# Performance work log

Measured on AMD Instinct MI355X. Metric: run time of the kernel, lower is better.

The kernel has to match this reference:

```python
import jax, jax.numpy as jnp
import numpy as np

N, F, H, E, ES, G = 50000, 64, 4, 300000, 400000, 128
NS, EPS = 0.2, 1e-5  # LeakyReLU slope, BN eps


def setup_inputs() -> dict:
    k = jax.random.split(jax.random.key(0), 16)
    rn = lambda i, s, sc=1.0: jax.random.normal(k[i], s, jnp.float32) * sc
    return {
        "x": rn(0, (N, F)),
        "edge_index": jax.random.randint(k[1], (2, E), 0, N),
        "batch": jnp.sort(jax.random.randint(k[2], (N,), 0, G)),
        "scatter_edge_index": jax.random.randint(k[3], (4, 2, ES), 0, N),
        "scatter_edge_attr": rn(4, (4, ES), 0.1),
        "gat_W": rn(5, (4, F, H * F), 0.05),
        "gat_asrc": rn(6, (4, H, F), 0.05),
        "gat_adst": rn(7, (4, H, F), 0.05),
        "gat_bias": jnp.zeros((4, H * F)),
        "mlp_W": rn(8, (4, H * F, F), 0.05),
        "mlp_b": jnp.zeros((4, F)),
        "mlp_g": jnp.ones((4, F)), "mlp_beta": jnp.zeros((4, F)),
        "mlp_rm": jnp.zeros((4, F)), "mlp_rv": jax.random.uniform(k[9], (4, F)) + 0.5,
        "fc1_W": rn(10, (F, 256), 0.05), "fc1_b": jnp.zeros((256,)),
        "fc1_g": jnp.ones((256,)), "fc1_beta": jnp.zeros((256,)),
        "fc1_rm": jnp.zeros((256,)), "fc1_rv": jax.random.uniform(k[11], (256,)) + 0.5,
        "fc2_W": rn(12, (256, 64), 0.05), "fc2_b": jnp.zeros((64,)),
        "fc2_g": jnp.ones((64,)), "fc2_beta": jnp.zeros((64,)),
        "fc2_rm": jnp.zeros((64,)), "fc2_rv": jax.random.uniform(k[13], (64,)) + 0.5,
        "fc3_W": rn(14, (64, 10), 0.05), "fc3_b": jnp.zeros((10,)),
        "fc3_g": jnp.ones((10,)), "fc3_beta": jnp.zeros((10,)),
        "fc3_rm": jnp.zeros((10,)), "fc3_rv": jax.random.uniform(k[15], (10,)) + 0.5,
    }


def _bn(h, g, b, rm, rv):
    # BatchNorm1d in eval mode (running stats)
    return g * (h - rm) * jax.lax.rsqrt(rv + EPS) + b


def _forward(floats, ints):
    (x, sea, gW, gas, gad, gb, mW, mb, mg, mbe, mrm, mrv,
     f1W, f1b, f1g, f1be, f1rm, f1rv, f2W, f2b, f2g, f2be, f2rm, f2rv,
     f3W, f3b, f3g, f3be, f3rm, f3rv) = floats
    edge_index, batch, sei = ints
    n = x.shape[0]
    loop = jnp.arange(n)
    src = jnp.concatenate([edge_index[0], loop])  # GATConv adds self-loops
    dst = jnp.concatenate([edge_index[1], loop])

    def solo(i, h):
        # edge_attr-weighted scatter-add (solo_pass, aggr='add')
        s, t = sei[i, 0], sei[i, 1]
        return jax.ops.segment_sum(sea[i][:, None] * h[s], t, num_segments=n)

    def gat_mlp(i, h):
        hh = (h @ gW[i]).reshape(n, H, F)                       # [N,H,F]
        e = (hh * gas[i]).sum(-1)[src] + (hh * gad[i]).sum(-1)[dst]  # [E+N,H]
        e = jnp.where(e > 0, e, NS * e)                         # LeakyReLU(0.2)
        m = jax.ops.segment_max(e, dst, num_segments=n)         # segment softmax over dst
        ex = jnp.exp(e - m[dst])
        ssum = jax.ops.segment_sum(ex, dst, num_segments=n)
        alpha = ex / ssum[dst]
        out = jax.ops.segment_sum(hh[src] * alpha[:, :, None], dst, num_segments=n)
        out = out.reshape(n, H * F) + gb[i]                     # concat heads + bias
        h2 = jax.nn.elu(out) @ mW[i] + mb[i]                    # ELU -> Dropout(eval) -> Linear
        return _bn(h2, mg[i], mbe[i], mrm[i], mrv[i])

    x0 = solo(0, x)
    xh = [jnp.abs(solo(i, x)) for i in (1, 2, 3)]
    branches = [x0] + [solo(0, h) for h in xh]
    branches = [gat_mlp(i, branches[i]) for i in range(4)]
    x_stage2 = x + branches[0] + branches[1] + branches[2] + branches[3]
    pooled = jax.ops.segment_sum(x_stage2, batch, num_segments=G)   # global_add_pool
    h = jax.nn.relu(_bn(pooled @ f1W + f1b, f1g, f1be, f1rm, f1rv))
    h = jax.nn.relu(_bn(h @ f2W + f2b, f2g, f2be, f2rm, f2rv))
    return _bn(h @ f3W + f3b, f3g, f3be, f3rm, f3rv)  # [G, num_classes]


def reference(x, edge_index, batch, scatter_edge_index, scatter_edge_attr, gat_W, gat_asrc, gat_adst, gat_bias, mlp_W, mlp_b, mlp_g, mlp_beta, mlp_rm, mlp_rv, fc1_W, fc1_b, fc1_g, fc1_beta, fc1_rm, fc1_rv, fc2_W, fc2_b, fc2_g, fc2_beta, fc2_rm, fc2_rv, fc3_W, fc3_b, fc3_g, fc3_beta, fc3_rm, fc3_rv):
    floats = (x, scatter_edge_attr, gat_W, gat_asrc, gat_adst, gat_bias, mlp_W, mlp_b, mlp_g, mlp_beta, mlp_rm, mlp_rv, fc1_W, fc1_b, fc1_g, fc1_beta, fc1_rm, fc1_rv, fc2_W, fc2_b, fc2_g, fc2_beta, fc2_rm, fc2_rv, fc3_W, fc3_b, fc3_g, fc3_beta, fc3_rm, fc3_rv)
    return _forward(floats, (edge_index, batch, scatter_edge_index))
```

## Files before the change

### kernel.cpp

```cpp
#include <hip/hip_runtime.h>

typedef unsigned int uint;
typedef unsigned short u16;

#define NN 50000
#define FF 64
#define NHD 4
#define EE 300000
#define ESN 400000
#define NG 128
#define NSLOPE 0.2f
#define EPSBN 1e-5f

#define BINSZ 64
#define NBIN 782
#define NPOS (NBIN * BINSZ)
#define CHUNK 2048
#define NBLK 196
#define BST 40
#define BCAP 38

typedef float f32x4 __attribute__((ext_vector_type(4)));
typedef float f32x2 __attribute__((ext_vector_type(2)));
typedef short bf16x8 __attribute__((ext_vector_type(8)));
union U8 { uint4 u; bf16x8 s; };

static __device__ __forceinline__ float lrelu(float e) {
  return fmaxf(e, NSLOPE * e);
}
static __device__ __forceinline__ float bl(uint u) {
  return __uint_as_float(u << 16);
}
static __device__ __forceinline__ float bh(uint u) {
  return __uint_as_float(u & 0xFFFF0000u);
}
static __device__ __forceinline__ uint f2bf(float f) {
  uint u = __float_as_uint(f);
  return (u + 0x7FFFu + ((u >> 16) & 1u)) >> 16;
}
static __device__ __forceinline__ uint packbf(float a, float b) {
  return f2bf(a) | (f2bf(b) << 16);
}

__global__ __launch_bounds__(256) void k_setup(
    const float2* __restrict__ x, const float* __restrict__ gW,
    const float* __restrict__ gas, const float* __restrict__ gad,
    const float* __restrict__ mW, const float* __restrict__ mb,
    const float* __restrict__ mg, const float* __restrict__ mbe,
    const float* __restrict__ mrm, const float* __restrict__ mrv,
    uint* __restrict__ xbf, uint* __restrict__ WB2, float* __restrict__ wasd,
    uint* __restrict__ MB, float* __restrict__ cvec) {
  int i = blockIdx.x * 256 + threadIdx.x;
  if (i < NN * 32) {
    float2 v = x[i];
    xbf[i] = packbf(v.x, v.y);
  }
  int t = i;
  if (t < 8192) {
    int b = t >> 11, id = t & 2047;
    int h = id >> 9, r2 = id & 511;
    int q2 = r2 >> 8, r3 = r2 & 255;
    int ct = r3 >> 6, l = r3 & 63;
    int c = h * 64 + ct * 16 + (l & 15);
    int k0 = q2 * 32 + (l >> 4) * 8;
    const float* Wp = gW + b * 16384;
    uint4 o;
    o.x = packbf(Wp[(k0 + 0) * 256 + c], Wp[(k0 + 1) * 256 + c]);
    o.y = packbf(Wp[(k0 + 2) * 256 + c], Wp[(k0 + 3) * 256 + c]);
    o.z = packbf(Wp[(k0 + 4) * 256 + c], Wp[(k0 + 5) * 256 + c]);
    o.w = packbf(Wp[(k0 + 6) * 256 + c], Wp[(k0 + 7) * 256 + c]);
    ((uint4*)WB2)[t] = o;
  } else if (t < 8192 + 2048) {
    int id = t - 8192;
    int b = id >> 9, r = id & 511;
    int sd = r >> 8, r2 = r & 255;
    int h = r2 >> 6, k = r2 & 63;
    const float* Wp = gW + b * 16384;
    const float* ap = (sd ? gad : gas) + b * 256 + h * 64;
    float acc = 0.f;
    for (int f = 0; f < 64; ++f) acc += Wp[k * 256 + h * 64 + f] * ap[f];
    wasd[((b * 2 + sd) * 4 + h) * 64 + k] = acc;
  } else if (t < 8192 + 2048 + 8192) {
    int id = t - 10240;
    int b = id >> 11, rem = id & 2047;
    int tt = rem >> 6, l = rem & 63;
    int tile = tt >> 3, q2 = tt & 7;
    int c = tile * 16 + (l & 15);
    int k0 = q2 * 32 + (l >> 4) * 8;
    const float* Mp = mW + b * 16384;
    float sc = mg[b * 64 + c] * rsqrtf(mrv[b * 64 + c] + EPSBN);
    float v[8];
#pragma unroll
    for (int j = 0; j < 8; ++j) v[j] = Mp[(k0 + j) * 64 + c] * sc;
    uint4 o;
    o.x = packbf(v[0], v[1]); o.y = packbf(v[2], v[3]);
    o.z = packbf(v[4], v[5]); o.w = packbf(v[6], v[7]);
    ((uint4*)MB)[id] = o;
  } else if (t < 8192 + 2048 + 8192 + 64) {
    int c = t - 18432;
    float acc = 0.f;
#pragma unroll
    for (int b = 0; b < 4; ++b) {
      float sc = mg[b * 64 + c] * rsqrtf(mrv[b * 64 + c] + EPSBN);
      acc += sc * (mb[b * 64 + c] - mrm[b * 64 + c]) + mbe[b * 64 + c];
    }
    cvec[c] = acc;
  }
}

__global__ __launch_bounds__(256) void k_sort1(
    const int* __restrict__ sei, const float* __restrict__ sea,
    const int* __restrict__ ei, uint2* __restrict__ sorted,
    u16* __restrict__ offs) {
  __shared__ uint hist[NBIN];
  __shared__ uint wsum[4];
  __shared__ __align__(16) uint2 buf[CHUNK];
  int y = blockIdx.y, blk = blockIdx.x, tid = threadIdx.x;
  int E = (y < 4) ? ESN : EE;
  int e0 = blk * CHUNK;
  if (e0 >= E) return;
  int ec = E - e0; if (ec > CHUNK) ec = CHUNK;
  for (int i = tid; i < NBIN; i += 256) hist[i] = 0;
  __syncthreads();
  const int* sptr; const int* tptr; const float* wptr = 0;
  if (y < 4) {
    sptr = sei + (size_t)y * 2 * ESN; tptr = sptr + ESN;
    wptr = sea + (size_t)y * ESN;
  } else {
    sptr = ei; tptr = ei + EE;
  }
  uint2 rec[8]; uint rbin[8];
#pragma unroll
  for (int k = 0; k < 8; ++k) {
    int idx = tid + k * 256;
    rbin[k] = 0xFFFFFFFFu;
    if (idx < ec) {
      int e = e0 + idx;
      int s = sptr[e], t = tptr[e];
      uint w = (y < 4) ? (f2bf(wptr[e]) << 16) : 0u;
      rec[k].x = (uint)s | ((uint)(t & 63) << 16);
      rec[k].y = w;
      rbin[k] = (uint)(t >> 6);
      atomicAdd(&hist[rbin[k]], 1u);
    }
  }
  __syncthreads();
  int t4 = tid * 4;
  uint h0 = 0, h1 = 0, h2 = 0, h3 = 0;
  if (t4 + 0 < NBIN) h0 = hist[t4 + 0];
  if (t4 + 1 < NBIN) h1 = hist[t4 + 1];
  if (t4 + 2 < NBIN) h2 = hist[t4 + 2];
  if (t4 + 3 < NBIN) h3 = hist[t4 + 3];
  uint sl = h0 + h1 + h2 + h3;
  uint pre = sl;
#pragma unroll
  for (int off = 1; off < 64; off <<= 1) {
    uint nv = __shfl_up(pre, off);
    if ((tid & 63) >= off) pre += nv;
  }
  int wid = tid >> 6;
  if ((tid & 63) == 63) wsum[wid] = pre;
  __syncthreads();
  uint wbase = 0;
#pragma unroll
  for (int w = 0; w < 4; ++w) if (w < wid) wbase += wsum[w];
  uint base = wbase + pre - sl;
  if (t4 + 0 < NBIN) hist[t4 + 0] = base;
  if (t4 + 1 < NBIN) hist[t4 + 1] = base + h0;
  if (t4 + 2 < NBIN) hist[t4 + 2] = base + h0 + h1;
  if (t4 + 3 < NBIN) hist[t4 + 3] = base + h0 + h1 + h2;
  __syncthreads();
  u16* ob = offs + ((size_t)y * NBLK + blk) * 784;
  for (int i = tid; i < NBIN; i += 256) ob[i] = (u16)hist[i];
  if (tid == 0) { ob[NBIN] = (u16)ec; ob[NBIN + 1] = (u16)ec; }
  __syncthreads();
#pragma unroll
  for (int k = 0; k < 8; ++k) {
    if (rbin[k] != 0xFFFFFFFFu) {
      uint p = atomicAdd(&hist[rbin[k]], 1u);
      buf[p] = rec[k];
    }
  }
  __syncthreads();
  uint2* sb = sorted + ((size_t)y * NBLK + blk) * CHUNK;
  uint4* s4 = (uint4*)sb;
  const uint4* b4 = (const uint4*)buf;
  int n4 = (ec + 1) >> 1;
  for (int i = tid; i < n4; i += 256) s4[i] = b4[i];
}

__global__ __launch_bounds__(256) void k_sort2(
    const u16* __restrict__ offs, const uint2* __restrict__ sorted,
    uint* __restrict__ pbk, uint* __restrict__ gbk) {
  __shared__ __align__(16) uint Lb[BINSZ * BST];
  __shared__ uint Lc[BINSZ];
  __shared__ uint dh[64], dpos[64], sperm[64];
  int y = blockIdx.y, bin = blockIdx.x, tid = threadIdx.x;
  if (tid < BINSZ) Lc[tid] = 0u;
  if (tid < 64) dh[tid] = 0u;
  __syncthreads();
  int nblk = (y < 4) ? NBLK : 147;
  for (int sb = tid; sb < nblk; sb += 256) {
    const u16* ob = offs + ((size_t)y * NBLK + sb) * 784;
    uint st = ob[bin], en = ob[bin + 1];
    const uint2* src = sorted + ((size_t)y * NBLK + sb) * CHUNK;
    for (uint i = st; i < en; ++i) {
      uint2 r = src[i];
      uint tl = (r.x >> 16) & 63u;
      uint p = atomicAdd(&Lc[tl], 1u);
      if (p < BCAP) Lb[tl * BST + 2 + p] = (r.x & 0xFFFFu) | r.y;
    }
  }
  __syncthreads();
  uint myd = 0;
  if (tid < 64) {
    myd = Lc[tid]; if (myd > 63u) myd = 63u;
    atomicAdd(&dh[63u - myd], 1u);
  }
  __syncthreads();
  if (tid < 64) {
    uint v = dh[tid], p = v;
#pragma unroll
    for (int off = 1; off < 64; off <<= 1) {
      uint nv = __shfl_up(p, off);
      if (tid >= off) p += nv;
    }
    dpos[tid] = p - v;
  }
  __syncthreads();
  if (tid < 64) {
    uint slot = atomicAdd(&dpos[63u - myd], 1u);
    sperm[slot] = (uint)tid;
    Lb[tid * BST + 0] = Lc[tid];
    Lb[tid * BST + 1] = (uint)(bin * BINSZ + tid);
  }
  __syncthreads();
  uint* out = (y < 4) ? (pbk + ((size_t)y * NPOS + (size_t)bin * BINSZ) * BST)
                      : (gbk + (size_t)bin * BINSZ * BST);
  uint4* o4v = (uint4*)out;
  for (int i = tid; i < 64 * (BST / 4); i += 256) {
    int pos = i / (BST / 4), q = i % (BST / 4);
    uint sn = sperm[pos];
    uint4 v = *(const uint4*)&Lb[sn * BST + q * 4];
    o4v[(size_t)pos * (BST / 4) + q] = v;
  }
}

__global__ __launch_bounds__(256) void k_solo_gA(
    const uint* __restrict__ xbf, const uint* __restrict__ pbk,
    const float* __restrict__ wasd, uint* __restrict__ bbuf,
    uint* __restrict__ tmpb, float* __restrict__ es4,
    float* __restrict__ ed4) {
  int i = blockIdx.y;
  int tid = threadIdx.x;
  int pos = blockIdx.x * 32 + (tid >> 3);
  int sl = tid & 7;
  const uint* bk = pbk + ((size_t)i * NPOS + pos) * BST;
  int deg = (int)bk[0]; deg = deg > BCAP ? BCAP : deg;
  int id = (int)bk[1];
  if (id >= NN) return;
  const uint* pp = bk + 2;
  f32x2 A0 = {0.f, 0.f}, A1 = {0.f, 0.f}, A2 = {0.f, 0.f}, A3 = {0.f, 0.f};
  for (int j = 0; j < deg; j += 4) {
    uint2 pa = *(const uint2*)&pp[j];
    uint2 pb = *(const uint2*)&pp[j + 2];
    uint p0 = pa.x;
    uint p1 = (j + 1 < deg) ? pa.y : 0u;
    uint p2 = (j + 2 < deg) ? pb.x : 0u;
    uint p3 = (j + 3 < deg) ? pb.y : 0u;
    uint4 v0 = *(const uint4*)&xbf[(size_t)(p0 & 0xFFFFu) * 32 + sl * 4];
    uint4 v1 = *(const uint4*)&xbf[(size_t)(p1 & 0xFFFFu) * 32 + sl * 4];
    uint4 v2 = *(const uint4*)&xbf[(size_t)(p2 & 0xFFFFu) * 32 + sl * 4];
    uint4 v3 = *(const uint4*)&xbf[(size_t)(p3 & 0xFFFFu) * 32 + sl * 4];
#define SOLOA_EDGE(V, W)                              \
    {                                                 \
      float w_ = (W);                                 \
      f32x2 w2_ = {w_, w_};                           \
      A0 += (f32x2){bl(V.x), bh(V.x)} * w2_;          \
      A1 += (f32x2){bl(V.y), bh(V.y)} * w2_;          \
      A2 += (f32x2){bl(V.z), bh(V.z)} * w2_;          \
      A3 += (f32x2){bl(V.w), bh(V.w)} * w2_;          \
    }
    SOLOA_EDGE(v0, bh(p0));
    SOLOA_EDGE(v1, bh(p1));
    SOLOA_EDGE(v2, bh(p2));
    SOLOA_EDGE(v3, bh(p3));
#undef SOLOA_EDGE
  }
  uint4 o;
  o.x = packbf(A0[0], A0[1]); o.y = packbf(A1[0], A1[1]);
  o.z = packbf(A2[0], A2[1]); o.w = packbf(A3[0], A3[1]);
  uint* out = (i == 0) ? bbuf : (tmpb + (size_t)(i - 1) * NN * 32);
  *(uint4*)&out[(size_t)id * 32 + sl * 4] = o;
  if (i == 0) {
    float pv[8] = {A0[0], A0[1], A1[0], A1[1], A2[0], A2[1], A3[0], A3[1]};
    const float* wa = wasd;
    float r[8];
#pragma unroll
    for (int o8 = 0; o8 < 8; ++o8) {
      const float* w8 = wa + o8 * 64 + sl * 8;
      float a = 0.f;
#pragma unroll
      for (int j = 0; j < 8; ++j) a += pv[j] * w8[j];
      r[o8] = a;
    }
#pragma unroll
    for (int off = 1; off < 8; off <<= 1)
#pragma unroll
      for (int o8 = 0; o8 < 8; ++o8) r[o8] += __shfl_xor(r[o8], off);
    if (sl == 0) {
      *(float4*)&es4[(size_t)id * 4] = make_float4(r[0], r[1], r[2], r[3]);
      *(float4*)&ed4[(size_t)id * 4] = make_float4(r[4], r[5], r[6], r[7]);
    }
  }
}

__global__ __launch_bounds__(256) void k_solo_gB(
    const uint* __restrict__ tmpb, const uint* __restrict__ pbk,
    const float* __restrict__ wasd, uint* __restrict__ bbuf,
    float* __restrict__ es4, float* __restrict__ ed4) {
  int tid = threadIdx.x;
  int pos = blockIdx.x * 32 + (tid >> 3);
  int sl = tid & 7;
  const uint* bk = pbk + (size_t)pos * BST;
  int deg = (int)bk[0]; deg = deg > BCAP ? BCAP : deg;
  int id = (int)bk[1];
  if (id >= NN) return;
  const uint* pp = bk + 2;
  const uint* t0 = tmpb;
  const uint* t1 = tmpb + (size_t)NN * 32;
  const uint* t2 = tmpb + (size_t)2 * NN * 32;
  f32x2 A[3][4];
#pragma unroll
  for (int k = 0; k < 3; ++k)
#pragma unroll
    for (int c = 0; c < 4; ++c) A[k][c] = (f32x2){0.f, 0.f};
  for (int j = 0; j < deg; j += 2) {
    uint2 pe2 = *(const uint2*)&pp[j];
    if (j + 1 >= deg) pe2.y = 0u;
    size_t ro0 = (size_t)(pe2.x & 0xFFFFu) * 32 + sl * 4;
    size_t ro1 = (size_t)(pe2.y & 0xFFFFu) * 32 + sl * 4;
    uint4 v00 = *(const uint4*)&t0[ro0];
    uint4 v01 = *(const uint4*)&t1[ro0];
    uint4 v02 = *(const uint4*)&t2[ro0];
    uint4 v10 = *(const uint4*)&t0[ro1];
    uint4 v11 = *(const uint4*)&t1[ro1];
    uint4 v12 = *(const uint4*)&t2[ro1];
    float w0 = bh(pe2.x), w1 = bh(pe2.y);
    f32x2 w20 = {w0, w0}, w21 = {w1, w1};
#define SOLOB_EDGE(K, V, W)                                       \
    {                                                             \
      A[K][0] += (f32x2){fabsf(bl(V.x)), fabsf(bh(V.x))} * (W);   \
      A[K][1] += (f32x2){fabsf(bl(V.y)), fabsf(bh(V.y))} * (W);   \
      A[K][2] += (f32x2){fabsf(bl(V.z)), fabsf(bh(V.z))} * (W);   \
      A[K][3] += (f32x2){fabsf(bl(V.w)), fabsf(bh(V.w))} * (W);   \
    }
    SOLOB_EDGE(0, v00, w20);
    SOLOB_EDGE(1, v01, w20);
    SOLOB_EDGE(2, v02, w20);
    SOLOB_EDGE(0, v10, w21);
    SOLOB_EDGE(1, v11, w21);
    SOLOB_EDGE(2, v12, w21);
#undef SOLOB_EDGE
  }
#pragma unroll
  for (int k = 0; k < 3; ++k) {
    int b = k + 1;
    uint4 o;
    o.x = packbf(A[k][0][0], A[k][0][1]); o.y = packbf(A[k][1][0], A[k][1][1]);
    o.z = packbf(A[k][2][0], A[k][2][1]); o.w = packbf(A[k][3][0], A[k][3][1]);
    *(uint4*)&bbuf[(size_t)b * NN * 32 + (size_t)id * 32 + sl * 4] = o;
    float pv[8] = {A[k][0][0], A[k][0][1], A[k][1][0], A[k][1][1],
                   A[k][2][0], A[k][2][1], A[k][3][0], A[k][3][1]};
    const float* wa = wasd + b * 512;
    float r[8];
#pragma unroll
    for (int o8 = 0; o8 < 8; ++o8) {
      const float* w8 = wa + o8 * 64 + sl * 8;
      float a = 0.f;
#pragma unroll
      for (int j = 0; j < 8; ++j) a += pv[j] * w8[j];
      r[o8] = a;
    }
#pragma unroll
    for (int off = 1; off < 8; off <<= 1)
#pragma unroll
      for (int o8 = 0; o8 < 8; ++o8) r[o8] += __shfl_xor(r[o8], off);
    if (sl == 0) {
      *(float4*)&es4[(size_t)b * NN * 4 + (size_t)id * 4] =
          make_float4(r[0], r[1], r[2], r[3]);
      *(float4*)&ed4[(size_t)b * NN * 4 + (size_t)id * 4] =
          make_float4(r[4], r[5], r[6], r[7]);
    }
  }
}

__global__ __launch_bounds__(256) void k_agg(
    const uint* __restrict__ gbk, const float* __restrict__ es4,
    const float* __restrict__ ed4, const uint* __restrict__ bbuf,
    uint* __restrict__ agg4) {
  __shared__ uint gbr[32][40];
  __shared__ uint2 meta[32][32];
  int br = blockIdx.y;
  const float4* es44 = (const float4*)(es4 + (size_t)br * NN * 4);
  const float4* ed44 = (const float4*)(ed4 + (size_t)br * NN * 4);
  const uint* bbf = bbuf + (size_t)br * NN * 32;
  int tid = threadIdx.x;
  int p0 = blockIdx.x * 32;
  for (int idx = tid; idx < 320; idx += 256) {
    int i = idx / 10, q = idx % 10;
    *(uint4*)&gbr[i][q * 4] =
        *(const uint4*)&gbk[((size_t)p0 + i) * BST + q * 4];
  }
  __syncthreads();
  {
    int g = tid >> 5, hl = tid & 31;
#pragma unroll
    for (int rep = 0; rep < 4; ++rep) {
      int i = rep * 8 + g;
      int id = (int)gbr[i][1];
      bool vld = id < NN;
      int nds = vld ? id : 0;
      int deg = vld ? (int)gbr[i][0] : 0;
      deg = deg > 31 ? 31 : deg;
      int s0 = (hl < deg) ? (int)gbr[i][2 + hl] : nds;
      bool act = hl <= deg;
      float4 edd = ed44[nds];
      float4 e4 = es44[s0];
      float val[4];
      val[0] = act ? lrelu(e4.x + edd.x) : -3e38f;
      val[1] = act ? lrelu(e4.y + edd.y) : -3e38f;
      val[2] = act ? lrelu(e4.z + edd.z) : -3e38f;
      val[3] = act ? lrelu(e4.w + edd.w) : -3e38f;
      float m[4] = {val[0], val[1], val[2], val[3]};
#pragma unroll
      for (int off = 1; off < 32; off <<= 1)
#pragma unroll
        for (int h = 0; h < 4; ++h) m[h] = fmaxf(m[h], __shfl_xor(m[h], off));
      float e[4], sm[4];
#pragma unroll
      for (int h = 0; h < 4; ++h) {
        e[h] = act ? __expf(val[h] - m[h]) : 0.f;
        sm[h] = e[h];
      }
#pragma unroll
      for (int off = 1; off < 32; off <<= 1)
#pragma unroll
        for (int h = 0; h < 4; ++h) sm[h] += __shfl_xor(sm[h], off);
      meta[i][hl] = make_uint2(packbf(e[0] / sm[0], e[1] / sm[1]),
                               packbf(e[2] / sm[2], e[3] / sm[3]));
    }
  }
  __syncthreads();
  {
    int wv = tid >> 6, l = tid & 63;
    int i = wv * 8 + (l >> 3), sl = l & 7;
    int id = (int)gbr[i][1];
    bool vld = id < NN;
    int self = vld ? id : 0;
    int deg = vld ? (int)gbr[i][0] : 0;
    deg = deg > 31 ? 31 : deg;
    int tot = deg + 1;
    f32x2 a00={0.f,0.f},a01={0.f,0.f},a02={0.f,0.f},a03={0.f,0.f};
    f32x2 a10={0.f,0.f},a11={0.f,0.f},a12={0.f,0.f},a13={0.f,0.f};
    f32x2 a20={0.f,0.f},a21={0.f,0.f},a22={0.f,0.f},a23={0.f,0.f};
    f32x2 a30={0.f,0.f},a31={0.f,0.f},a32={0.f,0.f},a33={0.f,0.f};
    for (int j = 0; j < tot; j += 4) {
      int s0 = (j     < deg) ? (int)gbr[i][2 + j]  : self;
      int s1 = (j + 1 < deg) ? (int)gbr[i][3 + j]  : self;
      int s2 = (j + 2 < deg) ? (int)gbr[i][4 + j]  : self;
      int s3 = (j + 3 < deg) ? (int)gbr[i][5 + j]  : self;
      uint2 al0 = meta[i][j];
      uint2 al1 = meta[i][j + 1];
      uint2 al2 = meta[i][j + 2];
      uint2 al3 = meta[i][j + 3];
      uint4 v0 = *(const uint4*)&bbf[(size_t)s0 * 32 + sl * 4];
      uint4 v1 = *(const uint4*)&bbf[(size_t)s1 * 32 + sl * 4];
      uint4 v2 = *(const uint4*)&bbf[(size_t)s2 * 32 + sl * 4];
      uint4 v3 = *(const uint4*)&bbf[(size_t)s3 * 32 + sl * 4];
#define AGG_EDGE(V, AL)                                              \
      {                                                              \
        f32x2 w0_={bl(AL.x),bl(AL.x)}, w1_={bh(AL.x),bh(AL.x)};      \
        f32x2 w2_={bl(AL.y),bl(AL.y)}, w3_={bh(AL.y),bh(AL.y)};      \
        f32x2 p0_={bl(V.x),bh(V.x)}, p1_={bl(V.y),bh(V.y)};          \
        f32x2 p2_={bl(V.z),bh(V.z)}, p3_={bl(V.w),bh(V.w)};          \
        a00+=p0_*w0_; a01+=p1_*w0_; a02+=p2_*w0_; a03+=p3_*w0_;      \
        a10+=p0_*w1_; a11+=p1_*w1_; a12+=p2_*w1_; a13+=p3_*w1_;      \
        a20+=p0_*w2_; a21+=p1_*w2_; a22+=p2_*w2_; a23+=p3_*w2_;      \
        a30+=p0_*w3_; a31+=p1_*w3_; a32+=p2_*w3_; a33+=p3_*w3_;      \
      }
      AGG_EDGE(v0, al0);
      AGG_EDGE(v1, al1);
      AGG_EDGE(v2, al2);
      AGG_EDGE(v3, al3);
#undef AGG_EDGE
    }
    if (vld) {
      uint* outp = agg4 + ((size_t)br * NN + id) * 128;
      uint4 o;
      o.x=packbf(a00[0],a00[1]); o.y=packbf(a01[0],a01[1]);
      o.z=packbf(a02[0],a02[1]); o.w=packbf(a03[0],a03[1]);
      *(uint4*)&outp[0 * 32 + sl * 4] = o;
      o.x=packbf(a10[0],a10[1]); o.y=packbf(a11[0],a11[1]);
      o.z=packbf(a12[0],a12[1]); o.w=packbf(a13[0],a13[1]);
      *(uint4*)&outp[1 * 32 + sl * 4] = o;
      o.x=packbf(a20[0],a20[1]); o.y=packbf(a21[0],a21[1]);
      o.z=packbf(a22[0],a22[1]); o.w=packbf(a23[0],a23[1]);
      *(uint4*)&outp[2 * 32 + sl * 4] = o;
      o.x=packbf(a30[0],a30[1]); o.y=packbf(a31[0],a31[1]);
      o.z=packbf(a32[0],a32[1]); o.w=packbf(a33[0],a33[1]);
      *(uint4*)&outp[3 * 32 + sl * 4] = o;
    }
  }
}

__global__ __launch_bounds__(256) void k_mlp2(
    const uint* __restrict__ agg4, const uint* __restrict__ WB2,
    const uint* __restrict__ MB4, const float* __restrict__ gb,
    const float* __restrict__ cvec, const float* __restrict__ xsrc,
    float* __restrict__ xs2) {
  __shared__ union UU2 {
    uint elu[4][32][32];
    float red[4][32][64];
  } u;
  int tid = threadIdx.x, wv = tid >> 6, l = tid & 63;
  int quad = l >> 4, m16 = l & 15;
  int n0 = blockIdx.x * 32;
  int h = wv;
  f32x4 macc[2][4] = {{{0.f,0.f,0.f,0.f},{0.f,0.f,0.f,0.f},
                       {0.f,0.f,0.f,0.f},{0.f,0.f,0.f,0.f}},
                      {{0.f,0.f,0.f,0.f},{0.f,0.f,0.f,0.f},
                       {0.f,0.f,0.f,0.f},{0.f,0.f,0.f,0.f}}};
  u16* eluw = (u16*)&u.elu[wv][0][0];
  for (int br = 0; br < 4; ++br) {
    uint4 Bh[2][4];
#pragma unroll
    for (int kk = 0; kk < 2; ++kk)
#pragma unroll
      for (int ct = 0; ct < 4; ++ct)
        Bh[kk][ct] =
            ((const uint4*)WB2)[(((br * 4 + h) * 2 + kk) * 4 + ct) * 64 + l];
#pragma unroll
    for (int mt = 0; mt < 2; ++mt) {
      int node = n0 + mt * 16 + m16;
      const uint* ap = agg4 + ((size_t)br * NN + node) * 128 + h * 32;
      U8 a0, a1;
      a0.u = *(const uint4*)&ap[quad * 4];
      a1.u = *(const uint4*)&ap[16 + quad * 4];
#pragma unroll
      for (int ct = 0; ct < 4; ++ct) {
        f32x4 acc = {0.f, 0.f, 0.f, 0.f};
        U8 b0, b1; b0.u = Bh[0][ct]; b1.u = Bh[1][ct];
        acc = __builtin_amdgcn_mfma_f32_16x16x32_bf16(a0.s, b0.s, acc, 0, 0, 0);
        acc = __builtin_amdgcn_mfma_f32_16x16x32_bf16(a1.s, b1.s, acc, 0, 0, 0);
        float gbv = gb[br * 256 + h * 64 + ct * 16 + m16];
#pragma unroll
        for (int r = 0; r < 4; ++r) {
          float v = acc[r] + gbv;
          v = v > 0.f ? v : (__expf(v) - 1.f);
          int row = mt * 16 + quad * 4 + r;
          int ucs = ((ct * 16 + m16) >> 1) ^ ((row & 7) << 2);
          eluw[(row * 32 + ucs) * 2 + (m16 & 1)] = (u16)f2bf(v);
        }
      }
    }
    const uint4* MBb = (const uint4*)MB4 + br * 2048;
    uint4 Bm[4][2];
#pragma unroll
    for (int t = 0; t < 4; ++t)
#pragma unroll
      for (int kk = 0; kk < 2; ++kk)
        Bm[t][kk] = MBb[(t * 8 + wv * 2 + kk) * 64 + l];
#pragma unroll
    for (int mt = 0; mt < 2; ++mt) {
      int row = mt * 16 + m16;
      int sw = (row & 7) << 2;
      const uint* er = &u.elu[wv][row][0];
      U8 a0, a1;
      a0.u = *(const uint4*)&er[(quad * 4) ^ sw];
      a1.u = *(const uint4*)&er[(16 + quad * 4) ^ sw];
#pragma unroll
      for (int t = 0; t < 4; ++t) {
        U8 b0, b1; b0.u = Bm[t][0]; b1.u = Bm[t][1];
        macc[mt][t] =
            __builtin_amdgcn_mfma_f32_16x16x32_bf16(a0.s, b0.s, macc[mt][t], 0, 0, 0);
        macc[mt][t] =
            __builtin_amdgcn_mfma_f32_16x16x32_bf16(a1.s, b1.s, macc[mt][t], 0, 0, 0);
      }
    }
  }
  __syncthreads();
#pragma unroll
  for (int mt = 0; mt < 2; ++mt)
#pragma unroll
    for (int t = 0; t < 4; ++t)
#pragma unroll
      for (int r = 0; r < 4; ++r)
        u.red[wv][mt * 16 + quad * 4 + r][t * 16 + m16] = macc[mt][t][r];
  __syncthreads();
  for (int e = tid; e < 2048; e += 256) {
    int node = e >> 6, col = e & 63;
    int nd = n0 + node;
    if (nd < NN) {
      float v = u.red[0][node][col] + u.red[1][node][col] +
                u.red[2][node][col] + u.red[3][node][col];
      size_t idx = (size_t)nd * 64 + col;
      xs2[idx] = xsrc[idx] + v + cvec[col];
    }
  }
}

__global__ __launch_bounds__(256) void k_poolhead(
    const float* __restrict__ xs2, const int* __restrict__ batch,
    const float* __restrict__ f1W, const float* __restrict__ f1b,
    const float* __restrict__ f1g, const float* __restrict__ f1be,
    const float* __restrict__ f1rm, const float* __restrict__ f1rv,
    const float* __restrict__ f2W, const float* __restrict__ f2b,
    const float* __restrict__ f2g, const float* __restrict__ f2be,
    const float* __restrict__ f2rm, const float* __restrict__ f2rv,
    const float* __restrict__ f3W, const float* __restrict__ f3b,
    const float* __restrict__ f3g, const float* __restrict__ f3be,
    const float* __restrict__ f3rm, const float* __restrict__ f3rv,
    float* __restrict__ out) {
  __shared__ float p[64], h1[256], h2[64], red[4][64];
  int g = blockIdx.x, tid = threadIdx.x;
  int wv = tid >> 6, lane = tid & 63;
  int lo = 0, hi = NN;
  while (lo < hi) { int mid = (lo + hi) >> 1; if (batch[mid] < g) lo = mid + 1; else hi = mid; }
  int beg = lo;
  lo = 0; hi = NN;
  while (lo < hi) { int mid = (lo + hi) >> 1; if (batch[mid] < g + 1) lo = mid + 1; else hi = mid; }
  int end = lo;
  float acc = 0.f;
  for (int n = beg + wv; n < end; n += 4) acc += xs2[(size_t)n * FF + lane];
  red[wv][lane] = acc;
  __syncthreads();
  if (tid < 64) p[tid] = red[0][tid] + red[1][tid] + red[2][tid] + red[3][tid];
  __syncthreads();
  {
    float a = f1b[tid];
    for (int k = 0; k < 64; ++k) a += p[k] * f1W[k * 256 + tid];
    a = f1g[tid] * (a - f1rm[tid]) * rsqrtf(f1rv[tid] + EPSBN) + f1be[tid];
    h1[tid] = a > 0.f ? a : 0.f;
  }
  __syncthreads();
  if (tid < 64) {
    float b = f2b[tid];
    for (int k = 0; k < 256; ++k) b += h1[k] * f2W[k * 64 + tid];
    b = f2g[tid] * (b - f2rm[tid]) * rsqrtf(f2rv[tid] + EPSBN) + f2be[tid];
    h2[tid] = b > 0.f ? b : 0.f;
  }
  __syncthreads();
  if (tid < 10) {
    float c = f3b[tid];
    for (int k = 0; k < 64; ++k) c += h2[k] * f3W[k * 10 + tid];
    c = f3g[tid] * (c - f3rm[tid]) * rsqrtf(f3rv[tid] + EPSBN) + f3be[tid];
    out[g * 10 + tid] = c;
  }
}

extern "C" void kernel_launch(void* const* d_in, const int* in_sizes, int n_in,
                              void* d_out, int out_size, void* d_ws,
                              size_t ws_size, hipStream_t stream) {
  const float* x     = (const float*)d_in[0];
  const int*   ei    = (const int*)d_in[1];
  const int*   batch = (const int*)d_in[2];
  const int*   sei   = (const int*)d_in[3];
  const float* sea   = (const float*)d_in[4];
  const float* gW    = (const float*)d_in[5];
  const float* gas   = (const float*)d_in[6];
  const float* gad   = (const float*)d_in[7];
  const float* gb    = (const float*)d_in[8];
  const float* mW    = (const float*)d_in[9];
  const float* mb    = (const float*)d_in[10];
  const float* mg    = (const float*)d_in[11];
  const float* mbe   = (const float*)d_in[12];
  const float* mrm   = (const float*)d_in[13];
  const float* mrv   = (const float*)d_in[14];
  const float* f1W   = (const float*)d_in[15];
  const float* f1b   = (const float*)d_in[16];
  const float* f1g   = (const float*)d_in[17];
  const float* f1be  = (const float*)d_in[18];
  const float* f1rm  = (const float*)d_in[19];
  const float* f1rv  = (const float*)d_in[20];
  const float* f2W   = (const float*)d_in[21];
  const float* f2b   = (const float*)d_in[22];
  const float* f2g   = (const float*)d_in[23];
  const float* f2be  = (const float*)d_in[24];
  const float* f2rm  = (const float*)d_in[25];
  const float* f2rv  = (const float*)d_in[26];
  const float* f3W   = (const float*)d_in[27];
  const float* f3b   = (const float*)d_in[28];
  const float* f3g   = (const float*)d_in[29];
  const float* f3be  = (const float*)d_in[30];
  const float* f3rm  = (const float*)d_in[31];
  const float* f3rv  = (const float*)d_in[32];
  float* out = (float*)d_out;

  char* base = (char*)d_ws;
  float* xs2 = (float*)base;
  uint* gbk  = (uint*)(base + (size_t)NN * 64 * 4);
  uint* xbf  = gbk + (size_t)NPOS * BST;
  uint* bbuf = xbf + (size_t)NN * 32;
  uint* tmpb = bbuf + (size_t)4 * NN * 32;
  uint* pbk  = tmpb + (size_t)3 * NN * 32;
  uint2* sorted = (uint2*)(pbk + (size_t)4 * NPOS * BST);
  u16* offs = (u16*)(sorted + (size_t)5 * NBLK * CHUNK);
  uint* agg4 = (uint*)(offs + (size_t)5 * NBLK * 784);
  float* es4 = (float*)(agg4 + ((size_t)4 * NN + 32) * 128);
  float* ed4 = es4 + (size_t)4 * NN * 4;
  float* cvec = ed4 + (size_t)4 * NN * 4;
  float* wasd = cvec + 64;
  uint* WB2 = (uint*)(wasd + 2048);
  uint* MB4 = WB2 + 4 * 8192;

  size_t need = (size_t)((char*)(MB4 + 4 * 8192) - base);
  if (ws_size < need) return;

  k_setup<<<(NN * 32 + 255) / 256, 256, 0, stream>>>(
      (const float2*)x, gW, gas, gad, mW, mb, mg, mbe, mrm, mrv, xbf, WB2,
      wasd, MB4, cvec);

  dim3 gS1(NBLK, 5);
  k_sort1<<<gS1, 256, 0, stream>>>(sei, sea, ei, sorted, offs);
  dim3 gS2(NBIN, 5);
  k_sort2<<<gS2, 256, 0, stream>>>(offs, sorted, pbk, gbk);

  dim3 gA(NPOS / 32, 4);
  k_solo_gA<<<gA, 256, 0, stream>>>(xbf, pbk, wasd, bbuf, tmpb, es4, ed4);
  k_solo_gB<<<NPOS / 32, 256, 0, stream>>>(tmpb, pbk, wasd, bbuf, es4, ed4);

  dim3 gAg(NPOS / 32, 4);
  k_agg<<<gAg, 256, 0, stream>>>(gbk, es4, ed4, bbuf, agg4);
  k_mlp2<<<(NN + 31) / 32, 256, 0, stream>>>(agg4, WB2, MB4, gb, cvec, x, xs2);

  k_poolhead<<<NG, 256, 0, stream>>>(xs2, batch, f1W, f1b, f1g, f1be, f1rm,
                                     f1rv, f2W, f2b, f2g, f2be, f2rm, f2rv,
                                     f3W, f3b, f3g, f3be, f3rm, f3rv, out);
}
```

Before: 399.6 us.

## Unroll solo gathers wider, use rcp in softmax, stage MLP inputs in LDS

```diff
diff --git a/kernel.cpp b/kernel.cpp
--- a/kernel.cpp
+++ b/kernel.cpp
@@ -261,17 +261,27 @@
   if (id >= NN) return;
   const uint* pp = bk + 2;
   f32x2 A0 = {0.f, 0.f}, A1 = {0.f, 0.f}, A2 = {0.f, 0.f}, A3 = {0.f, 0.f};
-  for (int j = 0; j < deg; j += 4) {
+  for (int j = 0; j < deg; j += 8) {
     uint2 pa = *(const uint2*)&pp[j];
     uint2 pb = *(const uint2*)&pp[j + 2];
+    uint2 pc = *(const uint2*)&pp[j + 4];
+    uint2 pd = *(const uint2*)&pp[j + 6];
     uint p0 = pa.x;
     uint p1 = (j + 1 < deg) ? pa.y : 0u;
     uint p2 = (j + 2 < deg) ? pb.x : 0u;
     uint p3 = (j + 3 < deg) ? pb.y : 0u;
+    uint p4 = (j + 4 < deg) ? pc.x : 0u;
+    uint p5 = (j + 5 < deg) ? pc.y : 0u;
+    uint p6 = (j + 6 < deg) ? pd.x : 0u;
+    uint p7 = (j + 7 < deg) ? pd.y : 0u;
     uint4 v0 = *(const uint4*)&xbf[(size_t)(p0 & 0xFFFFu) * 32 + sl * 4];
     uint4 v1 = *(const uint4*)&xbf[(size_t)(p1 & 0xFFFFu) * 32 + sl * 4];
     uint4 v2 = *(const uint4*)&xbf[(size_t)(p2 & 0xFFFFu) * 32 + sl * 4];
     uint4 v3 = *(const uint4*)&xbf[(size_t)(p3 & 0xFFFFu) * 32 + sl * 4];
+    uint4 v4 = *(const uint4*)&xbf[(size_t)(p4 & 0xFFFFu) * 32 + sl * 4];
+    uint4 v5 = *(const uint4*)&xbf[(size_t)(p5 & 0xFFFFu) * 32 + sl * 4];
+    uint4 v6 = *(const uint4*)&xbf[(size_t)(p6 & 0xFFFFu) * 32 + sl * 4];
+    uint4 v7 = *(const uint4*)&xbf[(size_t)(p7 & 0xFFFFu) * 32 + sl * 4];
 #define SOLOA_EDGE(V, W)                              \
     {                                                 \
       float w_ = (W);                                 \
@@ -285,6 +295,10 @@
     SOLOA_EDGE(v1, bh(p1));
     SOLOA_EDGE(v2, bh(p2));
     SOLOA_EDGE(v3, bh(p3));
+    SOLOA_EDGE(v4, bh(p4));
+    SOLOA_EDGE(v5, bh(p5));
+    SOLOA_EDGE(v6, bh(p6));
+    SOLOA_EDGE(v7, bh(p7));
 #undef SOLOA_EDGE
   }
   uint4 o;
@@ -335,19 +349,31 @@
   for (int k = 0; k < 3; ++k)
 #pragma unroll
     for (int c = 0; c < 4; ++c) A[k][c] = (f32x2){0.f, 0.f};
-  for (int j = 0; j < deg; j += 2) {
-    uint2 pe2 = *(const uint2*)&pp[j];
-    if (j + 1 >= deg) pe2.y = 0u;
-    size_t ro0 = (size_t)(pe2.x & 0xFFFFu) * 32 + sl * 4;
-    size_t ro1 = (size_t)(pe2.y & 0xFFFFu) * 32 + sl * 4;
+  for (int j = 0; j < deg; j += 4) {
+    uint2 pa = *(const uint2*)&pp[j];
+    uint2 pb = *(const uint2*)&pp[j + 2];
+    uint p0 = pa.x;
+    uint p1 = (j + 1 < deg) ? pa.y : 0u;
+    uint p2 = (j + 2 < deg) ? pb.x : 0u;
+    uint p3 = (j + 3 < deg) ? pb.y : 0u;
+    size_t ro0 = (size_t)(p0 & 0xFFFFu) * 32 + sl * 4;
+    size_t ro1 = (size_t)(p1 & 0xFFFFu) * 32 + sl * 4;
+    size_t ro2 = (size_t)(p2 & 0xFFFFu) * 32 + sl * 4;
+    size_t ro3 = (size_t)(p3 & 0xFFFFu) * 32 + sl * 4;
     uint4 v00 = *(const uint4*)&t0[ro0];
     uint4 v01 = *(const uint4*)&t1[ro0];
     uint4 v02 = *(const uint4*)&t2[ro0];
     uint4 v10 = *(const uint4*)&t0[ro1];
     uint4 v11 = *(const uint4*)&t1[ro1];
     uint4 v12 = *(const uint4*)&t2[ro1];
-    float w0 = bh(pe2.x), w1 = bh(pe2.y);
-    f32x2 w20 = {w0, w0}, w21 = {w1, w1};
+    uint4 v20 = *(const uint4*)&t0[ro2];
+    uint4 v21 = *(const uint4*)&t1[ro2];
+    uint4 v22 = *(const uint4*)&t2[ro2];
+    uint4 v30 = *(const uint4*)&t0[ro3];
+    uint4 v31 = *(const uint4*)&t1[ro3];
+    uint4 v32 = *(const uint4*)&t2[ro3];
+    float w0 = bh(p0), w1 = bh(p1), w2 = bh(p2), w3 = bh(p3);
+    f32x2 w20 = {w0, w0}, w21 = {w1, w1}, w22 = {w2, w2}, w23 = {w3, w3};
 #define SOLOB_EDGE(K, V, W)                                       \
     {                                                             \
       A[K][0] += (f32x2){fabsf(bl(V.x)), fabsf(bh(V.x))} * (W);   \
@@ -355,12 +381,10 @@
       A[K][2] += (f32x2){fabsf(bl(V.z)), fabsf(bh(V.z))} * (W);   \
       A[K][3] += (f32x2){fabsf(bl(V.w)), fabsf(bh(V.w))} * (W);   \
     }
-    SOLOB_EDGE(0, v00, w20);
-    SOLOB_EDGE(1, v01, w20);
-    SOLOB_EDGE(2, v02, w20);
-    SOLOB_EDGE(0, v10, w21);
-    SOLOB_EDGE(1, v11, w21);
-    SOLOB_EDGE(2, v12, w21);
+    SOLOB_EDGE(0, v00, w20); SOLOB_EDGE(1, v01, w20); SOLOB_EDGE(2, v02, w20);
+    SOLOB_EDGE(0, v10, w21); SOLOB_EDGE(1, v11, w21); SOLOB_EDGE(2, v12, w21);
+    SOLOB_EDGE(0, v20, w22); SOLOB_EDGE(1, v21, w22); SOLOB_EDGE(2, v22, w22);
+    SOLOB_EDGE(0, v30, w23); SOLOB_EDGE(1, v31, w23); SOLOB_EDGE(2, v32, w23);
 #undef SOLOB_EDGE
   }
 #pragma unroll
@@ -447,8 +471,11 @@
       for (int off = 1; off < 32; off <<= 1)
 #pragma unroll
         for (int h = 0; h < 4; ++h) sm[h] += __shfl_xor(sm[h], off);
-      meta[i][hl] = make_uint2(packbf(e[0] / sm[0], e[1] / sm[1]),
-                               packbf(e[2] / sm[2], e[3] / sm[3]));
+      float inv[4];
+#pragma unroll
+      for (int h = 0; h < 4; ++h) inv[h] = __builtin_amdgcn_rcpf(sm[h]);
+      meta[i][hl] = make_uint2(packbf(e[0] * inv[0], e[1] * inv[1]),
+                               packbf(e[2] * inv[2], e[3] * inv[3]));
     }
   }
   __syncthreads();
@@ -520,7 +547,10 @@
     const float* __restrict__ cvec, const float* __restrict__ xsrc,
     float* __restrict__ xs2) {
   __shared__ union UU2 {
-    uint elu[4][32][32];
+    struct {
+      uint astg[32][128];
+      uint elu[4][32][32];
+    } s;
     float red[4][32][64];
   } u;
   int tid = threadIdx.x, wv = tid >> 6, l = tid & 63;
@@ -531,8 +561,17 @@
                        {0.f,0.f,0.f,0.f},{0.f,0.f,0.f,0.f}},
                       {{0.f,0.f,0.f,0.f},{0.f,0.f,0.f,0.f},
                        {0.f,0.f,0.f,0.f},{0.f,0.f,0.f,0.f}}};
-  u16* eluw = (u16*)&u.elu[wv][0][0];
+  u16* eluw = (u16*)&u.s.elu[wv][0][0];
   for (int br = 0; br < 4; ++br) {
+    if (br) __syncthreads();
+    {
+      const uint* src = agg4 + ((size_t)br * NN + n0) * 128;
+      for (int i2 = tid; i2 < 4096; i2 += 256) {
+        int row = i2 >> 7, col = i2 & 127;
+        u.s.astg[row][col ^ ((row & 7) << 2)] = src[i2];
+      }
+    }
+    __syncthreads();
     uint4 Bh[2][4];
 #pragma unroll
     for (int kk = 0; kk < 2; ++kk)
@@ -542,11 +581,12 @@
             ((const uint4*)WB2)[(((br * 4 + h) * 2 + kk) * 4 + ct) * 64 + l];
 #pragma unroll
     for (int mt = 0; mt < 2; ++mt) {
-      int node = n0 + mt * 16 + m16;
-      const uint* ap = agg4 + ((size_t)br * NN + node) * 128 + h * 32;
+      int row = mt * 16 + m16;
+      const uint* ar = &u.s.astg[row][0];
+      int sw = (row & 7) << 2;
       U8 a0, a1;
-      a0.u = *(const uint4*)&ap[quad * 4];
-      a1.u = *(const uint4*)&ap[16 + quad * 4];
+      a0.u = *(const uint4*)&ar[(h * 32 + quad * 4) ^ sw];
+      a1.u = *(const uint4*)&ar[(h * 32 + 16 + quad * 4) ^ sw];
 #pragma unroll
       for (int ct = 0; ct < 4; ++ct) {
         f32x4 acc = {0.f, 0.f, 0.f, 0.f};
@@ -558,9 +598,9 @@
         for (int r = 0; r < 4; ++r) {
           float v = acc[r] + gbv;
           v = v > 0.f ? v : (__expf(v) - 1.f);
-          int row = mt * 16 + quad * 4 + r;
-          int ucs = ((ct * 16 + m16) >> 1) ^ ((row & 7) << 2);
-          eluw[(row * 32 + ucs) * 2 + (m16 & 1)] = (u16)f2bf(v);
+          int erow = mt * 16 + quad * 4 + r;
+          int ucs = ((ct * 16 + m16) >> 1) ^ ((erow & 7) << 2);
+          eluw[(erow * 32 + ucs) * 2 + (m16 & 1)] = (u16)f2bf(v);
         }
       }
     }
@@ -575,7 +615,7 @@
     for (int mt = 0; mt < 2; ++mt) {
       int row = mt * 16 + m16;
       int sw = (row & 7) << 2;
-      const uint* er = &u.elu[wv][row][0];
+      const uint* er = &u.s.elu[wv][row][0];
       U8 a0, a1;
       a0.u = *(const uint4*)&er[(quad * 4) ^ sw];
       a1.u = *(const uint4*)&er[(16 + quad * 4) ^ sw];
```

Result: no change. 392.8 us (-1.7%).
